# Performance work log

Measured on AMD Instinct MI355X. Metric: run time of the kernel, lower is better.

## Reference

```python
import jax, jax.numpy as jnp
import numpy as np

V, E, HD, H, T = 50000, 256, 512, 256, 50  # vocab, embed, hidden_dim, per-direction hidden, tagset
B, S = 128, 512


def setup_inputs() -> dict:
    key = jax.random.key(0)
    ks = jax.random.split(key, 16)
    def n(k, shape, s=0.05):
        return jax.random.normal(k, shape, dtype=jnp.float32) * s
    return {
        "sentences": jax.random.randint(ks[0], (B, S), 0, V),
        "tags": jax.random.randint(ks[1], (B, S), 0, T),
        "mask": jnp.ones((B, S), dtype=bool),
        "embedding": n(ks[2], (V, E), 0.1),
        "w_ih_f": n(ks[3], (4 * H, E)), "w_hh_f": n(ks[4], (4 * H, H)),
        "b_ih_f": n(ks[5], (4 * H,)), "b_hh_f": n(ks[6], (4 * H,)),
        "w_ih_b": n(ks[7], (4 * H, E)), "w_hh_b": n(ks[8], (4 * H, H)),
        "b_ih_b": n(ks[9], (4 * H,)), "b_hh_b": n(ks[10], (4 * H,)),
        "W_out": n(ks[11], (T, HD)), "b_out": n(ks[12], (T,)),
        "start_trans": n(ks[13], (T,), 0.1),
        "end_trans": n(ks[14], (T,), 0.1),
        "trans": n(ks[15], (T, T), 0.1),
    }


def _lstm(xs, w_ih, w_hh, b, reverse):
    # xs: [S, B, E]; PyTorch gate order i, f, g, o
    Hn = w_hh.shape[1]
    def cell(carry, xt):
        h, c = carry
        g = xt @ w_ih.T + h @ w_hh.T + b
        i, f, gg, o = jnp.split(g, 4, axis=-1)
        c = jax.nn.sigmoid(f) * c + jax.nn.sigmoid(i) * jnp.tanh(gg)
        h = jax.nn.sigmoid(o) * jnp.tanh(c)
        return (h, c), h
    z = jnp.zeros((xs.shape[1], Hn), xs.dtype)
    _, hs = jax.lax.scan(cell, (z, z), xs, reverse=reverse)
    return hs  # [S, B, Hn], time-aligned with xs


def reference(sentences, tags, mask, embedding, w_ih_f, w_hh_f, b_ih_f, b_hh_f,
              w_ih_b, w_hh_b, b_ih_b, b_hh_b, W_out, b_out,
              start_trans, end_trans, trans):
    xs = jnp.swapaxes(embedding[sentences], 0, 1)           # [S, B, E]
    hf = _lstm(xs, w_ih_f, w_hh_f, b_ih_f + b_hh_f, False)
    hb = _lstm(xs, w_ih_b, w_hh_b, b_ih_b + b_hh_b, True)
    emis = jnp.concatenate([hf, hb], -1) @ W_out.T + b_out  # [S, B, T]

    tagsT = jnp.swapaxes(tags, 0, 1)                        # [S, B]
    maskT = jnp.swapaxes(mask, 0, 1)                        # [S, B] bool
    mT = maskT.astype(emis.dtype)

    # --- numerator: score of the gold path (first timestep always on, per torchcrf) ---
    emit = jnp.take_along_axis(emis, tagsT[..., None], axis=-1)[..., 0]   # [S, B]
    num = start_trans[tagsT[0]] + emit[0]
    num = num + jnp.sum((trans[tagsT[:-1], tagsT[1:]] + emit[1:]) * mT[1:], axis=0)
    last = jnp.sum(maskT.astype(jnp.int32), axis=0) - 1                    # [B]
    num = num + end_trans[tags[jnp.arange(tags.shape[0]), last]]

    # --- denominator: log-partition via forward algorithm (logsumexp scan) ---
    alpha0 = start_trans[None, :] + emis[0]                 # [B, T]
    def step(alpha, inp):
        e_t, m_t = inp
        nxt = jax.nn.logsumexp(alpha[:, :, None] + trans[None] + e_t[:, None, :], axis=1)
        return jnp.where(m_t[:, None], nxt, alpha), None
    alpha, _ = jax.lax.scan(step, alpha0, (emis[1:], maskT[1:]))
    logZ = jax.nn.logsumexp(alpha + end_trans[None, :], axis=1)

    # model returns -crf(...) with reduction='mean'
    return -jnp.mean(num - logZ)
```

## Files before the change

kernel.cpp:

```cpp
#include <hip/hip_runtime.h>

typedef __bf16 bf16x8 __attribute__((ext_vector_type(8)));
typedef float f32x4 __attribute__((ext_vector_type(4)));
typedef float f32x2 __attribute__((ext_vector_type(2)));
typedef int i32x8 __attribute__((ext_vector_type(8)));
typedef unsigned short ushort_t;
typedef unsigned int u32x4 __attribute__((ext_vector_type(4)));
typedef long i64_t;

constexpr int Ee = 256;
constexpr int HDd = 512;
constexpr int Hh = 256;
constexpr int Tt = 50;
constexpr int Bb = 128;
constexpr int Ss = 512;
constexpr int G4 = 1024;
constexpr int SB = Ss * Bb;
constexpr int Tc = 64;
constexpr int NP = Ss / Tc;
constexpr int HSTR = 272;

constexpr float LOG2E = 1.4426950408889634f;
constexpr float K2f = 2.8853900817779268f;

#define DI __device__ __forceinline__

DI float bf2f(ushort_t u) {
    unsigned int x = ((unsigned int)u) << 16;
    return __builtin_bit_cast(float, x);
}
DI ushort_t f2bf(float f) {
    unsigned int x = __builtin_bit_cast(unsigned int, f);
    x += 0x7fffu + ((x >> 16) & 1u);
    return (ushort_t)(x >> 16);
}
DI bf16x8 cvt8(const float* p) {
    bf16x8 r;
#pragma unroll
    for (int i = 0; i < 8; ++i) r[i] = (__bf16)p[i];
    return r;
}
DI unsigned int pk4_fp8(float a, float b, float c, float d) {
    int v = __builtin_amdgcn_cvt_pk_fp8_f32(a, b, 0, false);
    v = __builtin_amdgcn_cvt_pk_fp8_f32(c, d, v, true);
    return (unsigned int)v;
}
DI unsigned char fp8_1(float a) {
    return (unsigned char)(__builtin_amdgcn_cvt_pk_fp8_f32(a, 0.f, 0, false) & 0xff);
}
DI float rcpf(float x) { return __builtin_amdgcn_rcpf(x); }

#if __has_builtin(__builtin_amdgcn_exp2f)
DI float ex2(float x) { return __builtin_amdgcn_exp2f(x); }
DI float ex2n(float x) { return __builtin_amdgcn_exp2f(-x); }
#else
DI float ex2(float x) {
    float r;
    asm("v_exp_f32 %0, %1\n\ts_nop 0" : "=v"(r) : "v"(x));
    return r;
}
DI float ex2n(float x) {
    float r;
    asm("v_exp_f32 %0, -%1\n\ts_nop 0" : "=v"(r) : "v"(x));
    return r;
}
#endif

DI void lds_barrier() {
    asm volatile("" ::: "memory");
    __builtin_amdgcn_s_waitcnt(0xC07F);
    __builtin_amdgcn_s_barrier();
    asm volatile("" ::: "memory");
}

__global__ void k_prep(const float* __restrict__ wihf, const float* __restrict__ whhf,
                       const float* __restrict__ wihb, const float* __restrict__ whhb,
                       const float* __restrict__ wout,
                       const float* __restrict__ bihf, const float* __restrict__ bhhf,
                       const float* __restrict__ bihb, const float* __restrict__ bhhb,
                       ushort_t* __restrict__ Wihf, ushort_t* __restrict__ Wihb,
                       unsigned char* __restrict__ Whhf8, unsigned char* __restrict__ Whhb8,
                       unsigned char* __restrict__ Wout8,
                       float* __restrict__ biasf, float* __restrict__ biasb,
                       unsigned int* __restrict__ flags) {
    int i = blockIdx.x * 256 + threadIdx.x;
    if (i < G4 * Ee) {
        float s = (((i >> 16) & 3) == 2) ? K2f : LOG2E;
        Wihf[i] = f2bf(wihf[i] * s);
        Wihb[i] = f2bf(wihb[i] * s);
    }
    if (i < G4 * Hh / 4) {
        int base = i * 4;
        float s = (((i >> 14) & 3) == 2) ? K2f : LOG2E;
        ((unsigned int*)Whhf8)[i] = pk4_fp8(whhf[base] * s, whhf[base + 1] * s,
                                            whhf[base + 2] * s, whhf[base + 3] * s);
        ((unsigned int*)Whhb8)[i] = pk4_fp8(whhb[base] * s, whhb[base + 1] * s,
                                            whhb[base + 2] * s, whhb[base + 3] * s);
    }
    if (i < 64 * HDd) Wout8[i] = 0;
    if (i < Tt * HDd) Wout8[i] = fp8_1(wout[i]);
    if (i < G4) {
        float s = (((i >> 8) & 3) == 2) ? K2f : LOG2E;
        biasf[i] = (bihf[i] + bhhf[i]) * s;
        biasb[i] = (bihb[i] + bhhb[i]) * s;
    }
    if (i < 16) flags[i] = 0;
}

struct PhaseArgs {
    const int* sentences;
    const float* emb;
    const ushort_t* Wihf;
    const ushort_t* Wihb;
    const float* biasf;
    const float* biasb;
    const unsigned char* Whhf8;
    const unsigned char* Whhb8;
    unsigned char* Gbuf;
    unsigned char* Hcat8;
    unsigned int* flags;
};

__global__ __launch_bounds__(1024, 4) void k_phase(PhaseArgs a) {
    __shared__ unsigned char hring[8][16][HSTR];
    const size_t CH = (size_t)Tc * Bb * G4;
    int blk = blockIdx.x;
    int tid = threadIdx.x;

    if (blk < 16) {
        int ln = tid & 15, qd = (tid >> 4) & 3, w = tid >> 6;
        int dir = blk >> 3;
        int b0 = (blk & 7) * 16;
        const unsigned char* Whh8 = dir ? a.Whhb8 : a.Whhf8;
        int jc0 = w * 16 + ln;

        i32x8 wreg[4][2];
#pragma unroll
        for (int g = 0; g < 4; ++g) {
            const unsigned char* wb = Whh8 + (size_t)(g * Hh + jc0) * Hh;
#pragma unroll
            for (int ks = 0; ks < 2; ++ks)
                wreg[g][ks] = *(const i32x8*)(wb + ks * 128 + qd * 32);
        }
        for (int i = tid; i < 8 * 16 * HSTR; i += 1024) ((unsigned char*)hring)[i] = 0;
        __syncthreads();
        float creg[4] = {};
        int sctr = 0;

        for (int p = 0; p < NP; ++p) {
            if (tid == 0) {
                while (__hip_atomic_load(&a.flags[p], __ATOMIC_RELAXED,
                                         __HIP_MEMORY_SCOPE_AGENT) < 240u)
                    __builtin_amdgcn_s_sleep(1);
                __threadfence();
            }
            __syncthreads();

            const unsigned char* G = a.Gbuf + ((size_t)(dir * 2 + (p & 1))) * CH;
            int goff = ((dir ? (Tc - 1) : 0) * Bb + b0) * G4 + jc0 * 4;
            const int gstep = dir ? -(Bb * G4) : (Bb * G4);

            unsigned int guA[4], guB[4];
#pragma unroll
            for (int reg = 0; reg < 4; ++reg)
                guA[reg] = *(const unsigned int*)(G + goff + (qd * 4 + reg) * G4);

            auto lstm_step = [&](unsigned int(&gcur)[4], unsigned int(&gnxt)[4], int step) {
                int rslot = (sctr + 7) & 7, wslot = sctr & 7;
                int goff2 = goff + gstep;
                if (step + 1 < Tc) {
#pragma unroll
                    for (int reg = 0; reg < 4; ++reg)
                        gnxt[reg] = *(const unsigned int*)(G + goff2 + (qd * 4 + reg) * G4);
                }
                i32x8 av2[2];
#pragma unroll
                for (int ks = 0; ks < 2; ++ks)
                    av2[ks] = *(const i32x8*)&hring[rslot][ln][ks * 128 + qd * 32];
                f32x4 acc[4];
#pragma unroll
                for (int reg = 0; reg < 4; ++reg) {
                    f32x2 lo = __builtin_amdgcn_cvt_pk_f32_fp8((int)gcur[reg], false);
                    f32x2 hi = __builtin_amdgcn_cvt_pk_f32_fp8((int)gcur[reg], true);
                    acc[0][reg] = lo[0];
                    acc[1][reg] = lo[1];
                    acc[2][reg] = hi[0];
                    acc[3][reg] = hi[1];
                }
#pragma unroll
                for (int ks = 0; ks < 2; ++ks)
#pragma unroll
                    for (int g = 0; g < 4; ++g)
                        acc[g] = __builtin_amdgcn_mfma_scale_f32_16x16x128_f8f6f4(
                            av2[ks], wreg[g][ks], acc[g],
                            0, 0,
                            0, 127,
                            0, 127);
#pragma unroll
                for (int reg = 0; reg < 4; ++reg) {
                    float ei = ex2n(acc[0][reg]);
                    float ef = ex2n(acc[1][reg]);
                    float eg = ex2(acc[2][reg]);
                    float eo = ex2n(acc[3][reg]);
                    float pf = 1.f + ef;
                    float pig = (1.f + ei) * (eg + 1.f);
                    float t2 = fmaf(eg, K2f, -K2f);
                    float cn = fmaf(creg[reg], pig, t2 * pf) * rcpf(pf * pig);
                    creg[reg] = cn;
                    float ec = ex2(cn);
                    float h = (ec - 1.f) * rcpf((1.f + eo) * (ec + 1.f));
                    hring[wslot][qd * 4 + reg][jc0] = fp8_1(h);
                }
                goff = goff2;
                lds_barrier();

                if ((sctr & 7) == 7) {
                    int tbase = sctr - 7;
                    int rid = tid >> 3;
                    int slot = rid >> 4, m = rid & 15;
                    int qp = tid & 7;
                    int t = dir ? (511 - (tbase + slot)) : (tbase + slot);
                    const unsigned char* src = &hring[slot][m][qp * 32];
                    unsigned char* dst = a.Hcat8 + ((size_t)(t * Bb + b0 + m)) * HDd + dir * Hh + qp * 32;
#pragma unroll
                    for (int i2 = 0; i2 < 2; ++i2) {
                        u32x4 v;
#pragma unroll
                        for (int k = 0; k < 4; ++k)
                            v[k] = *(const unsigned int*)(src + i2 * 16 + k * 4);
                        *(u32x4*)(dst + i2 * 16) = v;
                    }
                    lds_barrier();
                }
                ++sctr;
            };

            for (int step = 0; step < Tc; step += 2) {
                lstm_step(guA, guB, step);
                lstm_step(guB, guA, step + 1);
            }

            __syncthreads();
            if (tid == 0) atomicAdd(&a.flags[8 + p], 1u);
        }
    } else {
        int team = tid >> 8;
        int stid = tid & 255;
        int slot = (blk - 16) * 4 + team;
        int ln = stid & 15, qd = (stid >> 4) & 3, wv = stid >> 6;
        for (int q = 0; q < NP; ++q) {
            if (q >= 2) {
                if (tid == 0)
                    while (__hip_atomic_load(&a.flags[8 + q - 2], __ATOMIC_RELAXED,
                                             __HIP_MEMORY_SCOPE_AGENT) < 16u)
                        __builtin_amdgcn_s_sleep(64);
                __syncthreads();
            }
            for (int tile = slot; tile < 1024; tile += 960) {
                int dir = tile >> 9;
                int rem = tile & 511;
                int rt0 = rem >> 3, ct0 = rem & 7;
                const ushort_t* W = dir ? a.Wihb : a.Wihf;
                const float* bias = dir ? a.biasb : a.biasf;
                unsigned char* Gout = a.Gbuf + ((size_t)(dir * 2 + (q & 1))) * CH;
                int t0 = dir ? (NP - 1 - q) * Tc : q * Tc;
                int r0 = rt0 * 128 + (wv & 1) * 64;
                int n0 = ct0 * 128 + (wv >> 1) * 64;
                const float* aptr[4];
#pragma unroll
                for (int rt = 0; rt < 4; ++rt) {
                    int r = r0 + rt * 16 + ln;
                    int t = t0 + (r >> 7), b = r & 127;
                    aptr[rt] = a.emb + (size_t)a.sentences[b * Ss + t] * Ee;
                }
                int wrow[4];
#pragma unroll
                for (int ct = 0; ct < 4; ++ct) {
                    int c = n0 + ct * 16 + ln;
                    wrow[ct] = (c & 3) * 256 + (c >> 2);
                }
                f32x4 acc[4][4] = {};
                for (int ks = 0; ks < 8; ++ks) {
                    int k0 = ks * 32 + qd * 8;
                    bf16x8 av[4], bfr[4];
#pragma unroll
                    for (int rt = 0; rt < 4; ++rt) av[rt] = cvt8(aptr[rt] + k0);
#pragma unroll
                    for (int ct = 0; ct < 4; ++ct)
                        bfr[ct] = *(const bf16x8*)(W + (size_t)wrow[ct] * Ee + k0);
#pragma unroll
                    for (int rt = 0; rt < 4; ++rt)
#pragma unroll
                        for (int ct = 0; ct < 4; ++ct)
                            acc[rt][ct] = __builtin_amdgcn_mfma_f32_16x16x32_bf16(av[rt], bfr[ct], acc[rt][ct], 0, 0, 0);
                }
#pragma unroll
                for (int rt = 0; rt < 4; ++rt)
#pragma unroll
                    for (int ct = 0; ct < 4; ++ct) {
                        int c = n0 + ct * 16 + ln;
                        float bv = bias[wrow[ct]];
#pragma unroll
                        for (int reg = 0; reg < 4; ++reg) {
                            int row = r0 + rt * 16 + qd * 4 + reg;
                            Gout[(size_t)row * G4 + c] = fp8_1(acc[rt][ct][reg] + bv);
                        }
                    }
            }
            __syncthreads();
            if (tid == 0) {
                __threadfence();
                atomicAdd(&a.flags[q], 1u);
            }
        }
    }
}

__global__ __launch_bounds__(256, 2) void k_emis(const unsigned char* __restrict__ Hcat8,
                                                 const unsigned char* __restrict__ Wout8,
                                                 const float* __restrict__ bout,
                                                 float* __restrict__ emis) {
    int tid = threadIdx.x;
    int ln = tid & 15, qd = (tid >> 4) & 3, w = tid >> 6;
    int r0 = blockIdx.x * 128 + w * 32;
    f32x4 acc[2][4] = {};
    for (int ks = 0; ks < 16; ++ks) {
        int k0 = ks * 32 + qd * 8;
        i64_t av[2], bfr[4];
#pragma unroll
        for (int rt = 0; rt < 2; ++rt)
            av[rt] = *(const i64_t*)(Hcat8 + (size_t)(r0 + rt * 16 + ln) * HDd + k0);
#pragma unroll
        for (int ct = 0; ct < 4; ++ct)
            bfr[ct] = *(const i64_t*)(Wout8 + (size_t)(ct * 16 + ln) * HDd + k0);
#pragma unroll
        for (int rt = 0; rt < 2; ++rt)
#pragma unroll
            for (int ct = 0; ct < 4; ++ct)
                acc[rt][ct] = __builtin_amdgcn_mfma_f32_16x16x32_fp8_fp8(av[rt], bfr[ct], acc[rt][ct], 0, 0, 0);
    }
#pragma unroll
    for (int rt = 0; rt < 2; ++rt)
#pragma unroll
        for (int ct = 0; ct < 4; ++ct) {
            int j = ct * 16 + ln;
            if (j < Tt) {
                float bv = bout[j];
#pragma unroll
                for (int reg = 0; reg < 4; ++reg) {
                    int row = r0 + rt * 16 + qd * 4 + reg;
                    int t = row >> 7, b = row & 127;
                    emis[((size_t)b * Ss + t) * Tt + j] = acc[rt][ct][reg] + bv;
                }
            }
        }
}

__global__ __launch_bounds__(64) void k_crf(const float* __restrict__ emis,
                                            const float* __restrict__ start_trans,
                                            const float* __restrict__ end_trans,
                                            const float* __restrict__ trans,
                                            float* __restrict__ logZ) {
    __shared__ float E_s[64];
    int j = threadIdx.x;
    int b = blockIdx.x;
    const float* eb = emis + (size_t)b * Ss * Tt;

    float preg[52];
    preg[50] = 0.f;
    preg[51] = 0.f;
#pragma unroll
    for (int i = 0; i < Tt; ++i)
        preg[i] = (j < Tt) ? __expf(trans[i * Tt + j]) : 0.f;

    float astart = (j < Tt) ? (start_trans[j] + eb[j]) : 0.f;
    float a0 = __builtin_amdgcn_readfirstlane(astart);
    float vcur = (j < Tt) ? __expf(astart - a0) : 0.f;
    float logacc = a0;
    E_s[j] = vcur;

    float ecur[8], enxt[8];
#pragma unroll
    for (int i = 0; i < 8; ++i)
        ecur[i] = (j < Tt && 1 + i < Ss) ? eb[(1 + i) * Tt + j] : 0.f;

    for (int tb = 1; tb < Ss; tb += 8) {
#pragma unroll
        for (int i = 0; i < 8; ++i) {
            int tn = tb + 8 + i;
            enxt[i] = (j < Tt && tn < Ss) ? eb[(size_t)tn * Tt + j] : 0.f;
        }
        float ex[8];
#pragma unroll
        for (int i = 0; i < 8; ++i) ex[i] = __expf(ecur[i]);
#pragma unroll
        for (int i = 0; i < 8; ++i) {
            int t = tb + i;
            if (t >= Ss) break;
            float s0 = 0.f, s1 = 0.f, s2 = 0.f, s3 = 0.f;
#pragma unroll
            for (int i4 = 0; i4 < 13; ++i4) {
                f32x4 ev = *(const f32x4*)&E_s[i4 * 4];
                s0 = fmaf(ev[0], preg[i4 * 4 + 0], s0);
                s1 = fmaf(ev[1], preg[i4 * 4 + 1], s1);
                s2 = fmaf(ev[2], preg[i4 * 4 + 2], s2);
                s3 = fmaf(ev[3], preg[i4 * 4 + 3], s3);
            }
            vcur = ((s0 + s1) + (s2 + s3)) * ex[i];
            if (i == 3) {
                float n = __builtin_amdgcn_readfirstlane(vcur);
                vcur *= rcpf(n);
                logacc += __logf(n);
            }
            E_s[j] = vcur;
        }
        float n = __builtin_amdgcn_readfirstlane(vcur);
        vcur *= rcpf(n);
        E_s[j] = vcur;
        logacc += __logf(n);
#pragma unroll
        for (int i = 0; i < 8; ++i) ecur[i] = enxt[i];
    }
    float ve = (j < Tt) ? vcur * __expf(end_trans[j]) : 0.f;
    for (int off = 32; off > 0; off >>= 1) ve += __shfl_down(ve, off, 64);
    if (j == 0) logZ[b] = logacc + __logf(ve);
}

__global__ __launch_bounds__(256) void k_num(const int* __restrict__ tags,
                                             const float* __restrict__ emis,
                                             const float* __restrict__ trans,
                                             const float* __restrict__ start_trans,
                                             const float* __restrict__ end_trans,
                                             float* __restrict__ num) {
    __shared__ float red[4];
    int b = blockIdx.x, tid = threadIdx.x;
    const float* eb = emis + (size_t)b * Ss * Tt;
    float v = 0.f;
    for (int t = 1 + tid; t < Ss; t += 256) {
        int tp = tags[b * Ss + t - 1], tc = tags[b * Ss + t];
        v += trans[tp * Tt + tc] + eb[(size_t)t * Tt + tc];
    }
    if (tid == 0) {
        int t0 = tags[b * Ss + 0];
        v += start_trans[t0] + eb[t0] + end_trans[tags[b * Ss + Ss - 1]];
    }
    for (int off = 32; off > 0; off >>= 1) v += __shfl_down(v, off, 64);
    if ((tid & 63) == 0) red[tid >> 6] = v;
    __syncthreads();
    if (tid == 0) num[b] = red[0] + red[1] + red[2] + red[3];
}

__global__ __launch_bounds__(128) void k_out(const float* __restrict__ num,
                                             const float* __restrict__ logZ,
                                             float* __restrict__ out) {
    __shared__ float red[2];
    int b = threadIdx.x;
    float v = num[b] - logZ[b];
    for (int off = 32; off > 0; off >>= 1) v += __shfl_down(v, off, 64);
    if ((b & 63) == 0) red[b >> 6] = v;
    __syncthreads();
    if (b == 0) out[0] = -(red[0] + red[1]) / 128.f;
}

extern "C" void kernel_launch(void* const* d_in, const int* in_sizes, int n_in,
                              void* d_out, int out_size, void* d_ws, size_t ws_size,
                              hipStream_t stream) {
    const int* sentences = (const int*)d_in[0];
    const int* tags = (const int*)d_in[1];
    const float* emb = (const float*)d_in[3];
    const float* wihf = (const float*)d_in[4];
    const float* whhf = (const float*)d_in[5];
    const float* bihf = (const float*)d_in[6];
    const float* bhhf = (const float*)d_in[7];
    const float* wihb = (const float*)d_in[8];
    const float* whhb = (const float*)d_in[9];
    const float* bihb = (const float*)d_in[10];
    const float* bhhb = (const float*)d_in[11];
    const float* wout = (const float*)d_in[12];
    const float* bout = (const float*)d_in[13];
    const float* start_trans = (const float*)d_in[14];
    const float* end_trans = (const float*)d_in[15];
    const float* trans = (const float*)d_in[16];

    char* ws = (char*)d_ws;
    size_t off = 0;
    auto alloc = [&](size_t bytes) {
        void* p = ws + off;
        off += (bytes + 255) & ~(size_t)255;
        return p;
    };
    ushort_t* Wihf = (ushort_t*)alloc((size_t)G4 * Ee * 2);
    ushort_t* Wihb = (ushort_t*)alloc((size_t)G4 * Ee * 2);
    unsigned char* Whhf8 = (unsigned char*)alloc((size_t)G4 * Hh);
    unsigned char* Whhb8 = (unsigned char*)alloc((size_t)G4 * Hh);
    unsigned char* Wout8 = (unsigned char*)alloc((size_t)64 * HDd);
    float* biasf = (float*)alloc(G4 * 4);
    float* biasb = (float*)alloc(G4 * 4);
    unsigned char* Gbuf = (unsigned char*)alloc((size_t)4 * Tc * Bb * G4);
    unsigned char* Hcat8 = (unsigned char*)alloc((size_t)SB * HDd);
    float* emis = (float*)alloc((size_t)SB * Tt * 4);
    float* logZ = (float*)alloc(Bb * 4);
    float* num = (float*)alloc(Bb * 4);
    unsigned int* flags = (unsigned int*)alloc(64 * 4);
    (void)ws_size; (void)in_sizes; (void)n_in; (void)out_size;

    k_prep<<<dim3((G4 * Ee + 255) / 256), dim3(256), 0, stream>>>(
        wihf, whhf, wihb, whhb, wout, bihf, bhhf, bihb, bhhb,
        Wihf, Wihb, Whhf8, Whhb8, Wout8, biasf, biasb, flags);

    PhaseArgs pa;
    pa.sentences = sentences;
    pa.emb = emb;
    pa.Wihf = Wihf;
    pa.Wihb = Wihb;
    pa.biasf = biasf;
    pa.biasb = biasb;
    pa.Whhf8 = Whhf8;
    pa.Whhb8 = Whhb8;
    pa.Gbuf = Gbuf;
    pa.Hcat8 = Hcat8;
    pa.flags = flags;
    void* kargs[] = {&pa};
    hipLaunchCooperativeKernel((void*)k_phase, dim3(256), dim3(1024), kargs, 0, stream);

    k_emis<<<dim3(SB / 128), dim3(256), 0, stream>>>(Hcat8, Wout8, bout, emis);

    k_crf<<<dim3(Bb), dim3(64), 0, stream>>>(emis, start_trans, end_trans, trans, logZ);

    k_num<<<dim3(Bb), dim3(256), 0, stream>>>(tags, emis, trans, start_trans, end_trans, num);

    k_out<<<dim3(1), dim3(128), 0, stream>>>(num, logZ, (float*)d_out);
}
```

Before: 1.456 ms.

## Split each LSTM recurrence across two blocks with cross-block hidden-state exchange

Each LSTM batch tile is now handled by two 512-thread blocks, each computing half of the hidden units (128 columns), so the recurrent chain runs on 32 blocks instead of 16. The two blocks swap their hidden halves every timestep through a global buffer guarded by acquire/release counters. Each step now does two MFMA passes separated by an exchange and an extra barrier. The GEMM producer blocks are resized to 512 threads with two teams each. The aim is to shorten per-step latency by halving each block's work, at the cost of a global-memory handshake on the serial critical path every step.

```diff
diff --git a/kernel.cpp b/kernel.cpp
--- a/kernel.cpp
+++ b/kernel.cpp
@@ -20,6 +20,10 @@
 constexpr int NP = Ss / Tc;
 constexpr int HSTR = 272;
 
+constexpr int NLSTM = 32;
+constexpr int NGEMM = 256 - NLSTM;
+constexpr int GSLOTS = NGEMM * 2;
+
 constexpr float LOG2E = 1.4426950408889634f;
 constexpr float K2f = 2.8853900817779268f;
 
@@ -82,7 +86,7 @@
                        unsigned char* __restrict__ Whhf8, unsigned char* __restrict__ Whhb8,
                        unsigned char* __restrict__ Wout8,
                        float* __restrict__ biasf, float* __restrict__ biasb,
-                       unsigned int* __restrict__ flags) {
+                       unsigned int* __restrict__ flags, unsigned int* __restrict__ Hx) {
     int i = blockIdx.x * 256 + threadIdx.x;
     if (i < G4 * Ee) {
         float s = (((i >> 16) & 3) == 2) ? K2f : LOG2E;
@@ -104,7 +108,8 @@
         biasf[i] = (bihf[i] + bhhf[i]) * s;
         biasb[i] = (bihb[i] + bhhb[i]) * s;
     }
-    if (i < 16) flags[i] = 0;
+    if (i < 1024) flags[i] = 0;
+    if (i < NLSTM * 2 * 2048 / 4) Hx[i] = 0;
 }
 
 struct PhaseArgs {
@@ -118,21 +123,32 @@
     const unsigned char* Whhb8;
     unsigned char* Gbuf;
     unsigned char* Hcat8;
+    unsigned char* Hx;
     unsigned int* flags;
 };
 
-__global__ __launch_bounds__(1024, 4) void k_phase(PhaseArgs a) {
+__global__ __launch_bounds__(512, 2) void k_phase(PhaseArgs a) {
     __shared__ unsigned char hring[8][16][HSTR];
     const size_t CH = (size_t)Tc * Bb * G4;
     int blk = blockIdx.x;
     int tid = threadIdx.x;
 
-    if (blk < 16) {
+    if (blk < NLSTM) {
         int ln = tid & 15, qd = (tid >> 4) & 3, w = tid >> 6;
-        int dir = blk >> 3;
+        int dir = blk >> 4;
+        int half = (blk >> 3) & 1;
         int b0 = (blk & 7) * 16;
         const unsigned char* Whh8 = dir ? a.Whhb8 : a.Whhf8;
-        int jc0 = w * 16 + ln;
+        int jc0 = half * 128 + w * 16 + ln;
+
+        unsigned char* hx_out = a.Hx + (size_t)blk * 2 * 2048;
+        const unsigned char* hx_in = a.Hx + (size_t)(blk ^ 8) * 2 * 2048;
+        unsigned int* ctrX = &a.flags[16 + blk * 16];
+        unsigned int* ctrP = &a.flags[16 + (blk ^ 8) * 16];
+        int xrow = tid >> 5;
+        int xc4 = (tid & 31) * 4;
+        int obase = half * 128;
+        int pbase = obase ^ 128;
 
         i32x8 wreg[4][2];
 #pragma unroll
@@ -142,7 +158,7 @@
             for (int ks = 0; ks < 2; ++ks)
                 wreg[g][ks] = *(const i32x8*)(wb + ks * 128 + qd * 32);
         }
-        for (int i = tid; i < 8 * 16 * HSTR; i += 1024) ((unsigned char*)hring)[i] = 0;
+        for (int i = tid; i < 8 * 16 * HSTR; i += 512) ((unsigned char*)hring)[i] = 0;
         __syncthreads();
         float creg[4] = {};
         int sctr = 0;
@@ -150,7 +166,7 @@
         for (int p = 0; p < NP; ++p) {
             if (tid == 0) {
                 while (__hip_atomic_load(&a.flags[p], __ATOMIC_RELAXED,
-                                         __HIP_MEMORY_SCOPE_AGENT) < 240u)
+                                         __HIP_MEMORY_SCOPE_AGENT) < (unsigned)NGEMM)
                     __builtin_amdgcn_s_sleep(1);
                 __threadfence();
             }
@@ -168,15 +184,15 @@
             auto lstm_step = [&](unsigned int(&gcur)[4], unsigned int(&gnxt)[4], int step) {
                 int rslot = (sctr + 7) & 7, wslot = sctr & 7;
                 int goff2 = goff + gstep;
-                if (step + 1 < Tc) {
-#pragma unroll
-                    for (int reg = 0; reg < 4; ++reg)
-                        gnxt[reg] = *(const unsigned int*)(G + goff2 + (qd * 4 + reg) * G4);
-                }
-                i32x8 av2[2];
-#pragma unroll
-                for (int ks = 0; ks < 2; ++ks)
-                    av2[ks] = *(const i32x8*)&hring[rslot][ln][ks * 128 + qd * 32];
+
+                if (tid == 0) {
+                    while (__hip_atomic_load(ctrP, __ATOMIC_ACQUIRE,
+                                             __HIP_MEMORY_SCOPE_AGENT) < (unsigned)sctr) {}
+                }
+                lds_barrier();
+                unsigned int pv = *(const unsigned int*)(hx_in + ((sctr - 1) & 1) * 2048
+                                                         + xrow * 128 + xc4);
+                i32x8 av_own = *(const i32x8*)&hring[rslot][ln][obase + qd * 32];
                 f32x4 acc[4];
 #pragma unroll
                 for (int reg = 0; reg < 4; ++reg) {
@@ -188,14 +204,16 @@
                     acc[3][reg] = hi[1];
                 }
 #pragma unroll
-                for (int ks = 0; ks < 2; ++ks)
-#pragma unroll
-                    for (int g = 0; g < 4; ++g)
-                        acc[g] = __builtin_amdgcn_mfma_scale_f32_16x16x128_f8f6f4(
-                            av2[ks], wreg[g][ks], acc[g],
-                            0, 0,
-                            0, 127,
-                            0, 127);
+                for (int g = 0; g < 4; ++g)
+                    acc[g] = __builtin_amdgcn_mfma_scale_f32_16x16x128_f8f6f4(
+                        av_own, wreg[g][half], acc[g], 0, 0, 0, 127, 0, 127);
+                *(unsigned int*)&hring[rslot][xrow][pbase + xc4] = pv;
+                lds_barrier();
+                i32x8 av_p = *(const i32x8*)&hring[rslot][ln][pbase + qd * 32];
+#pragma unroll
+                for (int g = 0; g < 4; ++g)
+                    acc[g] = __builtin_amdgcn_mfma_scale_f32_16x16x128_f8f6f4(
+                        av_p, wreg[g][half ^ 1], acc[g], 0, 0, 0, 127, 0, 127);
 #pragma unroll
                 for (int reg = 0; reg < 4; ++reg) {
                     float ei = ex2n(acc[0][reg]);
@@ -211,17 +229,18 @@
                     float h = (ec - 1.f) * rcpf((1.f + eo) * (ec + 1.f));
                     hring[wslot][qd * 4 + reg][jc0] = fp8_1(h);
                 }
-                goff = goff2;
                 lds_barrier();
-
+                unsigned int ov = *(const unsigned int*)&hring[wslot][xrow][obase + xc4];
+                *(unsigned int*)(hx_out + (sctr & 1) * 2048 + xrow * 128 + xc4) = ov;
                 if ((sctr & 7) == 7) {
                     int tbase = sctr - 7;
-                    int rid = tid >> 3;
+                    int rid = tid >> 2;
                     int slot = rid >> 4, m = rid & 15;
-                    int qp = tid & 7;
+                    int qp = tid & 3;
                     int t = dir ? (511 - (tbase + slot)) : (tbase + slot);
-                    const unsigned char* src = &hring[slot][m][qp * 32];
-                    unsigned char* dst = a.Hcat8 + ((size_t)(t * Bb + b0 + m)) * HDd + dir * Hh + qp * 32;
+                    const unsigned char* src = &hring[slot][m][obase + qp * 32];
+                    unsigned char* dst = a.Hcat8 + ((size_t)(t * Bb + b0 + m)) * HDd
+                                         + dir * Hh + half * 128 + qp * 32;
 #pragma unroll
                     for (int i2 = 0; i2 < 2; ++i2) {
                         u32x4 v;
@@ -230,7 +249,16 @@
                             v[k] = *(const unsigned int*)(src + i2 * 16 + k * 4);
                         *(u32x4*)(dst + i2 * 16) = v;
                     }
-                    lds_barrier();
+                }
+                goff = goff2;
+                __syncthreads();
+                if (tid == 0)
+                    __hip_atomic_store(ctrX, (unsigned)(sctr + 1), __ATOMIC_RELEASE,
+                                       __HIP_MEMORY_SCOPE_AGENT);
+                if (step + 1 < Tc) {
+#pragma unroll
+                    for (int reg = 0; reg < 4; ++reg)
+                        gnxt[reg] = *(const unsigned int*)(G + goff + (qd * 4 + reg) * G4);
                 }
                 ++sctr;
             };
@@ -246,17 +274,17 @@
     } else {
         int team = tid >> 8;
         int stid = tid & 255;
-        int slot = (blk - 16) * 4 + team;
+        int slot = (blk - NLSTM) * 2 + team;
         int ln = stid & 15, qd = (stid >> 4) & 3, wv = stid >> 6;
         for (int q = 0; q < NP; ++q) {
             if (q >= 2) {
                 if (tid == 0)
                     while (__hip_atomic_load(&a.flags[8 + q - 2], __ATOMIC_RELAXED,
-                                             __HIP_MEMORY_SCOPE_AGENT) < 16u)
+                                             __HIP_MEMORY_SCOPE_AGENT) < (unsigned)NLSTM)
                         __builtin_amdgcn_s_sleep(64);
                 __syncthreads();
             }
-            for (int tile = slot; tile < 1024; tile += 960) {
+            for (int tile = slot; tile < 1024; tile += GSLOTS) {
                 int dir = tile >> 9;
                 int rem = tile & 511;
                 int rt0 = rem >> 3, ct0 = rem & 7;
@@ -501,12 +529,13 @@
     float* emis = (float*)alloc((size_t)SB * Tt * 4);
     float* logZ = (float*)alloc(Bb * 4);
     float* num = (float*)alloc(Bb * 4);
-    unsigned int* flags = (unsigned int*)alloc(64 * 4);
+    unsigned int* flags = (unsigned int*)alloc(4096);
+    unsigned char* Hx = (unsigned char*)alloc((size_t)NLSTM * 2 * 2048);
     (void)ws_size; (void)in_sizes; (void)n_in; (void)out_size;
 
     k_prep<<<dim3((G4 * Ee + 255) / 256), dim3(256), 0, stream>>>(
         wihf, whhf, wihb, whhb, wout, bihf, bhhf, bihb, bhhb,
-        Wihf, Wihb, Whhf8, Whhb8, Wout8, biasf, biasb, flags);
+        Wihf, Wihb, Whhf8, Whhb8, Wout8, biasf, biasb, flags, (unsigned int*)Hx);
 
     PhaseArgs pa;
     pa.sentences = sentences;
@@ -519,9 +548,10 @@
     pa.Whhb8 = Whhb8;
     pa.Gbuf = Gbuf;
     pa.Hcat8 = Hcat8;
+    pa.Hx = Hx;
     pa.flags = flags;
     void* kargs[] = {&pa};
-    hipLaunchCooperativeKernel((void*)k_phase, dim3(256), dim3(1024), kargs, 0, stream);
+    hipLaunchCooperativeKernel((void*)k_phase, dim3(256), dim3(512), kargs, 0, stream);
 
     k_emis<<<dim3(SB / 128), dim3(256), 0, stream>>>(Hcat8, Wout8, bout, emis);
 
```

Result: slower. 3.248 ms (+123.0%).
